# Kernel tuning notes

Hardware: AMD Instinct MI355X
Metric: run time of the kernel (lower is better)

Reference implementation:

```python
import jax, jax.numpy as jnp
import numpy as np

B, N, D = 8, 2048, 512


def setup_inputs() -> dict:
    key = jax.random.key(0)
    ks = jax.random.split(key, 8)
    s = 1.0 / np.sqrt(D)
    return {
        "x": jax.random.normal(ks[0], (B, N, D), dtype=jnp.float32),
        "event_lengths": jax.random.randint(ks[1], (B,), 1, N + 1, dtype=jnp.int64),
        "Wq": jax.random.uniform(ks[2], (D, D), jnp.float32, -s, s),
        "bq": jnp.zeros((D,), jnp.float32),
        "Wk": jax.random.uniform(ks[3], (D, D), jnp.float32, -s, s),
        "bk": jnp.zeros((D,), jnp.float32),
        "Wv": jax.random.uniform(ks[4], (D, D), jnp.float32, -s, s),
        "bv": jnp.zeros((D,), jnp.float32),
    }


def reference(x, event_lengths, Wq, bq, Wk, bk, Wv, bv):
    # x: [B, N, D]; linear layers follow torch convention y = x @ W^T + b
    q = jnp.einsum("bnd,ed->bne", x, Wq) + bq
    k = jnp.einsum("bnd,ed->bne", x, Wk) + bk
    v = jnp.einsum("bnd,ed->bne", x, Wv) + bv

    d = x.shape[-1]
    scores = jnp.einsum("bqd,bkd->bqk", q, k) / jnp.sqrt(jnp.asarray(d, jnp.float32))

    # per-sample padding mask: valid iff row < len AND col < len
    n = x.shape[1]
    idx = jnp.arange(n)
    L = event_lengths[:, None, None]  # [B,1,1]
    mask = (idx[None, :, None] < L) & (idx[None, None, :] < L)  # [B,N,N]
    scores = jnp.where(mask, scores, jnp.float32(-1e9))

    attn = jax.nn.softmax(scores, axis=-1)  # dropout omitted (eval mode)
    return jnp.einsum("bqk,bkd->bqd", attn, v)
```

## Files before the change

### kernel.cpp

```cpp
#include <hip/hip_runtime.h>

typedef _Float16 half8  __attribute__((ext_vector_type(8)));
typedef _Float16 half4  __attribute__((ext_vector_type(4)));
typedef _Float16 half2v __attribute__((ext_vector_type(2)));
typedef float    floatx4 __attribute__((ext_vector_type(4)));
typedef float    float4v __attribute__((ext_vector_type(4)));
typedef float    float2v __attribute__((ext_vector_type(2)));

#define BB 8
#define NN 2048
#define DD 512


#define WAITV(N)  asm volatile("s_waitcnt vmcnt(" #N ")" ::: "memory")
#define WAITL0()  asm volatile("s_waitcnt lgkmcnt(0)" ::: "memory")
#define BARRIER() asm volatile("s_barrier" ::: "memory")

__device__ __forceinline__ void stage_tile(const _Float16* __restrict__ g,
                                           int gstride, _Float16* lds,
                                           int w, int lane)
{
#pragma unroll
    for (int j = 0; j < 2; ++j) {
        int grp = w * 2 + j;
        int r   = grp * 16 + (lane >> 2);
        int cb  = (lane & 3) ^ ((r >> 1) & 3);
        const _Float16* gp = g + (size_t)r * gstride + cb * 8;
        _Float16* lp = lds + grp * 512;
        __builtin_amdgcn_global_load_lds(
            (const __attribute__((address_space(1))) void*)gp,
            (__attribute__((address_space(3))) void*)lp, 16, 0, 0);
    }
}

__device__ __forceinline__ void stage_tile64(const _Float16* __restrict__ g,
                                             int gstride, _Float16* lds,
                                             int w, int lane)
{
    int r  = w * 16 + (lane >> 2);
    int cb = (lane & 3) ^ ((r >> 1) & 3);
    const _Float16* gp = g + (size_t)r * gstride + cb * 8;
    _Float16* lp = lds + w * 512;
    __builtin_amdgcn_global_load_lds(
        (const __attribute__((address_space(1))) void*)gp,
        (__attribute__((address_space(3))) void*)lp, 16, 0, 0);
}

__device__ __forceinline__ half8 frag(const _Float16* tile, int m, int quad)
{
    return *(const half8*)&tile[m * 32 + ((quad ^ ((m >> 1) & 3)) * 8)];
}

__global__ __launch_bounds__(256) void prep_kernel(
    const float* __restrict__ x, const float* __restrict__ Wq,
    const float* __restrict__ Wk, const float* __restrict__ Wv,
    const int* __restrict__ lens,
    _Float16* __restrict__ xh, _Float16* __restrict__ wqh,
    _Float16* __restrict__ wkh, _Float16* __restrict__ wvh,
    float* __restrict__ sx)
{
    const int b  = blockIdx.y;
    const int n0 = blockIdx.x * 64;
    const int t  = threadIdx.x;
    const int Lp = (lens[b] + 127) & ~127;
    const float*   base  = x  + ((size_t)b * NN + n0) * DD + 2 * t;
    _Float16*      hbase = xh + ((size_t)b * NN + n0) * DD + 2 * t;

    int nw = Lp - n0;
    nw = nw < 0 ? 0 : (nw > 64 ? 64 : nw);

    float s0 = 0.f, s1 = 0.f;
    int n = 0;
    for (; n < nw; ++n) {
        float2v f = *(const float2v*)&base[(size_t)n * DD];
        s0 += f[0]; s1 += f[1];
        half2v h; h[0] = (_Float16)f[0]; h[1] = (_Float16)f[1];
        *(half2v*)&hbase[(size_t)n * DD] = h;
    }
    for (; n < 64; ++n) {
        float2v f = *(const float2v*)&base[(size_t)n * DD];
        s0 += f[0]; s1 += f[1];
    }
    atomicAdd(&sx[b * DD + 2 * t],     s0);
    atomicAdd(&sx[b * DD + 2 * t + 1], s1);

    const int gbid = b * 32 + blockIdx.x;
#pragma unroll
    for (int k = 0; k < 3; ++k) {
        int wi = gbid * 768 + k * 256 + t;
        const float* src; _Float16* dst; int i;
        if (wi < 65536)       { src = Wq; dst = wqh; i = wi; }
        else if (wi < 131072) { src = Wk; dst = wkh; i = wi - 65536; }
        else                  { src = Wv; dst = wvh; i = wi - 131072; }
        float4v f = *(const float4v*)&src[(size_t)i * 4];
        half4 h;
        for (int j = 0; j < 4; ++j) h[j] = (_Float16)f[j];
        *(half4*)&dst[(size_t)i * 4] = h;
    }
}

__global__ __launch_bounds__(256) void mvgemv_kernel(
    const float* __restrict__ Wv, const float* __restrict__ bv,
    const float* __restrict__ sx, float* __restrict__ mean_v)
{
    const int blk = blockIdx.x;
    const int b   = blk >> 7;
    const int e   = (blk & 127) * 4 + (threadIdx.x >> 6);
    const int lane = threadIdx.x & 63;
    const float* wr = Wv + (size_t)e * DD + lane * 8;
    const float* xr = sx + b * DD + lane * 8;
    float s = 0.f;
    for (int j = 0; j < 8; ++j) s += wr[j] * xr[j];
    for (int off = 32; off > 0; off >>= 1) s += __shfl_xor(s, off);
    if (lane == 0)
        mean_v[b * DD + e] = s * (1.0f / 2048.0f) + bv[e];
}

__global__ __launch_bounds__(256) void projqk_kernel(
    const _Float16* __restrict__ xh,
    const _Float16* __restrict__ wqh, const _Float16* __restrict__ wkh,
    const float* __restrict__ bq, const float* __restrict__ bk,
    const int* __restrict__ lens,
    _Float16* __restrict__ qb, _Float16* __restrict__ kb)
{
    const int z = blockIdx.z;
    const int r0 = blockIdx.y * 128;
    const int bb = r0 >> 11;
    if ((r0 & 2047) >= lens[bb]) return;
    const _Float16* Wh  = z ? wkh : wqh;
    const float*    bias= z ? bk  : bq;
    _Float16*       outp= z ? kb  : qb;
    const int c0 = blockIdx.x * 128;

    __shared__ __align__(16) _Float16 As[3][128 * 32];
    __shared__ __align__(16) _Float16 Bs[3][128 * 32];

    const int tid  = threadIdx.x;
    const int lane = tid & 63;
    const int w    = tid >> 6;
    const int wm   = w >> 1, wn = w & 1;
    const int lr   = lane & 15;
    const int quad = lane >> 4;

    floatx4 zero; zero[0]=0.f; zero[1]=0.f; zero[2]=0.f; zero[3]=0.f;
    floatx4 acc[4][4];
    for (int i = 0; i < 4; ++i)
        for (int j = 0; j < 4; ++j) acc[i][j] = zero;

    const _Float16* Abase = xh + (size_t)r0 * DD;
    const _Float16* Bbase = Wh + (size_t)c0 * DD;

    stage_tile(Abase +  0, DD, As[0], w, lane);
    stage_tile(Bbase +  0, DD, Bs[0], w, lane);
    stage_tile(Abase + 32, DD, As[1], w, lane);
    stage_tile(Bbase + 32, DD, Bs[1], w, lane);

    int cur = 0;
    for (int kt = 0; kt < 16; ++kt) {
        int nx = (kt + 2 < 16) ? kt + 2 : 15;
        int nb = cur + 2; if (nb >= 3) nb -= 3;
        stage_tile(Abase + nx * 32, DD, As[nb], w, lane);
        stage_tile(Bbase + nx * 32, DD, Bs[nb], w, lane);
        WAITV(8);
        BARRIER();
        half8 a[4], b[4];
        for (int mt = 0; mt < 4; ++mt) a[mt] = frag(As[cur], wm * 64 + mt * 16 + lr, quad);
        for (int nt = 0; nt < 4; ++nt) b[nt] = frag(Bs[cur], wn * 64 + nt * 16 + lr, quad);
        for (int mt = 0; mt < 4; ++mt)
            for (int nt = 0; nt < 4; ++nt)
                acc[mt][nt] = __builtin_amdgcn_mfma_f32_16x16x32_f16(a[mt], b[nt], acc[mt][nt], 0, 0, 0);
        WAITL0();
        BARRIER();
        cur = (cur + 1 == 3) ? 0 : cur + 1;
    }
    WAITV(0);

    for (int mt = 0; mt < 4; ++mt)
        for (int nt = 0; nt < 4; ++nt)
            for (int r = 0; r < 4; ++r) {
                int row = r0 + wm * 64 + mt * 16 + quad * 4 + r;
                int col = c0 + wn * 64 + nt * 16 + lr;
                outp[(size_t)row * DD + col] = (_Float16)(acc[mt][nt][r] + bias[col]);
            }
}

__global__ __launch_bounds__(256) void projv_kernel(
    const _Float16* __restrict__ xh,
    const _Float16* __restrict__ wvh, const float* __restrict__ bv,
    const int* __restrict__ lens, _Float16* __restrict__ vhT)
{
    const int b  = blockIdx.z;
    const int e0 = blockIdx.y * 128;
    const int n0 = blockIdx.x * 128;
    if (n0 >= lens[b]) return;

    __shared__ __align__(16) _Float16 As[3][128 * 32];
    __shared__ __align__(16) _Float16 Bs[3][128 * 32];

    const int tid  = threadIdx.x;
    const int lane = tid & 63;
    const int w    = tid >> 6;
    const int wm   = w >> 1, wn = w & 1;
    const int lr   = lane & 15;
    const int quad = lane >> 4;

    floatx4 zero; zero[0]=0.f; zero[1]=0.f; zero[2]=0.f; zero[3]=0.f;
    floatx4 acc[4][4];
    for (int i = 0; i < 4; ++i)
        for (int j = 0; j < 4; ++j) acc[i][j] = zero;

    const _Float16* Abase = wvh + (size_t)e0 * DD;
    const _Float16* Bbase = xh + ((size_t)b * NN + n0) * DD;

    stage_tile(Abase +  0, DD, As[0], w, lane);
    stage_tile(Bbase +  0, DD, Bs[0], w, lane);
    stage_tile(Abase + 32, DD, As[1], w, lane);
    stage_tile(Bbase + 32, DD, Bs[1], w, lane);

    int cur = 0;
    for (int kt = 0; kt < 16; ++kt) {
        int nx = (kt + 2 < 16) ? kt + 2 : 15;
        int nb = cur + 2; if (nb >= 3) nb -= 3;
        stage_tile(Abase + nx * 32, DD, As[nb], w, lane);
        stage_tile(Bbase + nx * 32, DD, Bs[nb], w, lane);
        WAITV(8);
        BARRIER();
        half8 a[4], bfr[4];
        for (int mt = 0; mt < 4; ++mt) a[mt]   = frag(As[cur], wm * 64 + mt * 16 + lr, quad);
        for (int nt = 0; nt < 4; ++nt) bfr[nt] = frag(Bs[cur], wn * 64 + nt * 16 + lr, quad);
        for (int mt = 0; mt < 4; ++mt)
            for (int nt = 0; nt < 4; ++nt)
                acc[mt][nt] = __builtin_amdgcn_mfma_f32_16x16x32_f16(a[mt], bfr[nt], acc[mt][nt], 0, 0, 0);
        WAITL0();
        BARRIER();
        cur = (cur + 1 == 3) ? 0 : cur + 1;
    }
    WAITV(0);

    for (int mt = 0; mt < 4; ++mt)
        for (int nt = 0; nt < 4; ++nt)
            for (int r = 0; r < 4; ++r) {
                int e = e0 + wm * 64 + mt * 16 + quad * 4 + r;
                int n = n0 + wn * 64 + nt * 16 + lr;
                vhT[((size_t)b * DD + e) * NN + n] = (_Float16)(acc[mt][nt][r] + bv[e]);
            }
}

__global__ __launch_bounds__(256) void scores_kernel(
    const _Float16* __restrict__ qb, const _Float16* __restrict__ kb,
    const int* __restrict__ lens, _Float16* __restrict__ S,
    float* __restrict__ rowsum)
{
    const int b  = blockIdx.z;
    const int r0 = blockIdx.y * 128;
    const int c0 = blockIdx.x * 128;
    const int L  = lens[b];
    if (r0 >= L || c0 >= L) return;
    const _Float16* Abase = qb + (size_t)b * NN * DD + (size_t)r0 * DD;
    const _Float16* Bbase = kb + (size_t)b * NN * DD + (size_t)c0 * DD;

    __shared__ __align__(16) _Float16 As[3][128 * 32];
    __shared__ __align__(16) _Float16 Bs[3][128 * 32];

    const int tid  = threadIdx.x;
    const int lane = tid & 63;
    const int w    = tid >> 6;
    const int wm   = w >> 1, wn = w & 1;
    const int lr   = lane & 15;
    const int quad = lane >> 4;

    floatx4 zero; zero[0]=0.f; zero[1]=0.f; zero[2]=0.f; zero[3]=0.f;
    floatx4 acc[4][4];
    for (int i = 0; i < 4; ++i)
        for (int j = 0; j < 4; ++j) acc[i][j] = zero;

    stage_tile(Abase +  0, DD, As[0], w, lane);
    stage_tile(Bbase +  0, DD, Bs[0], w, lane);
    stage_tile(Abase + 32, DD, As[1], w, lane);
    stage_tile(Bbase + 32, DD, Bs[1], w, lane);

    int cur = 0;
    for (int kt = 0; kt < 16; ++kt) {
        int nx = (kt + 2 < 16) ? kt + 2 : 15;
        int nb = cur + 2; if (nb >= 3) nb -= 3;
        stage_tile(Abase + nx * 32, DD, As[nb], w, lane);
        stage_tile(Bbase + nx * 32, DD, Bs[nb], w, lane);
        WAITV(8);
        BARRIER();
        half8 a[4], bfr[4];
        for (int mt = 0; mt < 4; ++mt) a[mt]   = frag(As[cur], wm * 64 + mt * 16 + lr, quad);
        for (int nt = 0; nt < 4; ++nt) bfr[nt] = frag(Bs[cur], wn * 64 + nt * 16 + lr, quad);
        for (int mt = 0; mt < 4; ++mt)
            for (int nt = 0; nt < 4; ++nt)
                acc[mt][nt] = __builtin_amdgcn_mfma_f32_16x16x32_f16(a[mt], bfr[nt], acc[mt][nt], 0, 0, 0);
        WAITL0();
        BARRIER();
        cur = (cur + 1 == 3) ? 0 : cur + 1;
    }
    WAITV(0);

    const float scale = 0.044194173824159216f;
    float psum[4][4];
    for (int mt = 0; mt < 4; ++mt)
        for (int r = 0; r < 4; ++r) psum[mt][r] = 0.f;

    for (int mt = 0; mt < 4; ++mt)
        for (int nt = 0; nt < 4; ++nt)
            for (int r = 0; r < 4; ++r) {
                int q    = r0 + wm * 64 + mt * 16 + quad * 4 + r;
                int kcol = c0 + wn * 64 + nt * 16 + lr;
                float e  = (kcol < L) ? __expf(acc[mt][nt][r] * scale) : 0.f;
                psum[mt][r] += e;
                S[((size_t)b * NN + q) * NN + kcol] = (_Float16)e;
            }

    for (int mt = 0; mt < 4; ++mt)
        for (int r = 0; r < 4; ++r) {
            float s = psum[mt][r];
            s += __shfl_xor(s, 1);
            s += __shfl_xor(s, 2);
            s += __shfl_xor(s, 4);
            s += __shfl_xor(s, 8);
            if (lr == 0) {
                int q = r0 + wm * 64 + mt * 16 + quad * 4 + r;
                if (q < L) atomicAdd(&rowsum[b * NN + q], s);
            }
        }
}

__global__ __launch_bounds__(256) void pv_kernel(
    const _Float16* __restrict__ P, const _Float16* __restrict__ vhT,
    const int* __restrict__ lens, const float* __restrict__ mean_v,
    const float* __restrict__ rowsum, float* __restrict__ out)
{
    const int b  = blockIdx.z;
    const int L  = lens[b];
    const int r0 = blockIdx.y * 64;
    const int c0 = blockIdx.x * 128;
    const int KT = (r0 < L) ? ((L + 31) >> 5) : 0;
    const _Float16* A  = P   + (size_t)b * NN * NN + (size_t)r0 * NN;
    const _Float16* Vh = vhT + (size_t)b * DD * NN + (size_t)c0 * NN;

    __shared__ __align__(16) _Float16 As[2][64 * 32];
    __shared__ __align__(16) _Float16 Bhs[2][128 * 32];

    const int tid  = threadIdx.x;
    const int lane = tid & 63;
    const int w    = tid >> 6;
    const int lr   = lane & 15;
    const int quad = lane >> 4;

    floatx4 zero; zero[0]=0.f; zero[1]=0.f; zero[2]=0.f; zero[3]=0.f;
    floatx4 acc[4][2];
    for (int i = 0; i < 4; ++i)
        for (int j = 0; j < 2; ++j) acc[i][j] = zero;

    if (KT > 0) {
        stage_tile64(A, NN, As[0], w, lane);
        stage_tile (Vh, NN, Bhs[0], w, lane);
    }
    for (int kt = 0; kt < KT; ++kt) {
        const int cur = kt & 1;
        __syncthreads();
        if (kt + 1 < KT) {
            stage_tile64(A + (size_t)(kt + 1) * 32, NN, As[cur ^ 1], w, lane);
            stage_tile (Vh + (size_t)(kt + 1) * 32, NN, Bhs[cur ^ 1], w, lane);
        }
        half8 a[4], bh[2];
        for (int mt = 0; mt < 4; ++mt) a[mt]  = frag(As[cur], mt * 16 + lr, quad);
        for (int nt = 0; nt < 2; ++nt) bh[nt] = frag(Bhs[cur], w * 32 + nt * 16 + lr, quad);
        for (int mt = 0; mt < 4; ++mt)
            for (int nt = 0; nt < 2; ++nt)
                acc[mt][nt] = __builtin_amdgcn_mfma_f32_16x16x32_f16(a[mt], bh[nt], acc[mt][nt], 0, 0, 0);
    }

    float mval[2];
    for (int nt = 0; nt < 2; ++nt)
        mval[nt] = mean_v[b * DD + c0 + w * 32 + nt * 16 + lr];

    for (int mt = 0; mt < 4; ++mt)
        for (int r = 0; r < 4; ++r) {
            int q = r0 + mt * 16 + quad * 4 + r;
            float inv = 0.f;
            if (q < L) inv = 1.0f / rowsum[b * NN + q];
            for (int nt = 0; nt < 2; ++nt) {
                int e = c0 + w * 32 + nt * 16 + lr;
                float val = (q < L) ? acc[mt][nt][r] * inv : mval[nt];
                out[((size_t)b * NN + q) * DD + e] = val;
            }
        }
}

extern "C" void kernel_launch(void* const* d_in, const int* in_sizes, int n_in,
                              void* d_out, int out_size, void* d_ws, size_t ws_size,
                              hipStream_t stream) {
    const float* x    = (const float*)d_in[0];
    const int*   lens = (const int*)d_in[1];
    const float* Wq   = (const float*)d_in[2];
    const float* bq   = (const float*)d_in[3];
    const float* Wk   = (const float*)d_in[4];
    const float* bk   = (const float*)d_in[5];
    const float* Wv   = (const float*)d_in[6];
    const float* bv   = (const float*)d_in[7];
    float* out = (float*)d_out;

    char* ws = (char*)d_ws;
    const size_t MB = 1024 * 1024;
    _Float16* qb  = (_Float16*)(ws);
    _Float16* kb  = (_Float16*)(ws + 16 * MB);
    _Float16* vh  = (_Float16*)(ws + 32 * MB);
    float*    mv  = (float*)   (ws + 48 * MB);
    float*    sx  = (float*)   (ws + 48 * MB + 64 * 1024);
    float*    rs  = (float*)   (ws + 48 * MB + 80 * 1024);
    _Float16* S   = (_Float16*)(ws + 64 * MB);
    _Float16* xh  = (_Float16*)(ws + 64 * MB);
    _Float16* wqh = (_Float16*)(ws + 80 * MB);
    _Float16* wkh = (_Float16*)(ws + 80 * MB + 512 * 1024);
    _Float16* wvh = (_Float16*)(ws + 81 * MB);

    hipMemsetAsync(sx, 0, BB * DD * sizeof(float) + BB * NN * sizeof(float), stream);
    prep_kernel  <<<dim3(32, 8),     256, 0, stream>>>(x, Wq, Wk, Wv, lens, xh, wqh, wkh, wvh, sx);
    mvgemv_kernel<<<1024,            256, 0, stream>>>(Wv, bv, sx, mv);
    projqk_kernel<<<dim3(4, 128, 2), 256, 0, stream>>>(xh, wqh, wkh, bq, bk, lens, qb, kb);
    projv_kernel <<<dim3(16, 4, 8),  256, 0, stream>>>(xh, wvh, bv, lens, vh);
    scores_kernel<<<dim3(16, 16, 8), 256, 0, stream>>>(qb, kb, lens, S, rs);
    pv_kernel    <<<dim3(4, 32, 8),  256, 0, stream>>>(S, vh, lens, mv, rs, out);
}
```

Baseline: 235.6 us.

## Split prep into flat cast and mean kernels, halve PV row tile

The fused prep kernel is split into a flat elementwise fp16 cast kernel over x and the weights, plus a separate column-sum kernel for the mean of x. Both spread across many more threads. The PV kernel row tile drops from 64 to 32 and the grid doubles, which raises parallelism for short sequences at the cost of re-reading V tiles more often. The scores epilogue is reorganised to keep the row-sum partials per m-tile, lowering register pressure. Because the cast and the mean each read x separately, x is now read twice from memory.

```diff
diff --git a/kernel.cpp b/kernel.cpp
--- a/kernel.cpp
+++ b/kernel.cpp
@@ -2,10 +2,8 @@
 
 typedef _Float16 half8  __attribute__((ext_vector_type(8)));
 typedef _Float16 half4  __attribute__((ext_vector_type(4)));
-typedef _Float16 half2v __attribute__((ext_vector_type(2)));
 typedef float    floatx4 __attribute__((ext_vector_type(4)));
 typedef float    float4v __attribute__((ext_vector_type(4)));
-typedef float    float2v __attribute__((ext_vector_type(2)));
 
 #define BB 8
 #define NN 2048
@@ -33,7 +31,7 @@
     }
 }
 
-__device__ __forceinline__ void stage_tile64(const _Float16* __restrict__ g,
+__device__ __forceinline__ void stage_tile16(const _Float16* __restrict__ g,
                                              int gstride, _Float16* lds,
                                              int w, int lane)
 {
@@ -56,47 +54,42 @@
     const float* __restrict__ Wk, const float* __restrict__ Wv,
     const int* __restrict__ lens,
     _Float16* __restrict__ xh, _Float16* __restrict__ wqh,
-    _Float16* __restrict__ wkh, _Float16* __restrict__ wvh,
-    float* __restrict__ sx)
+    _Float16* __restrict__ wkh, _Float16* __restrict__ wvh)
+{
+    const int XQ = (BB * NN * DD) / 4;
+    const int WQ = (DD * DD) / 4;
+    int t = blockIdx.x * 256 + threadIdx.x;
+    const float* src; _Float16* dst; int i;
+    if (t < XQ) {
+        int row = t >> 7;
+        int b   = row >> 11;
+        if ((row & 2047) >= ((lens[b] + 127) & ~127)) return;
+        src = x;  dst = xh;  i = t;
+    }
+    else if (t < XQ + WQ)   { src = Wq; dst = wqh; i = t - XQ; }
+    else if (t < XQ + 2*WQ) { src = Wk; dst = wkh; i = t - XQ - WQ; }
+    else if (t < XQ + 3*WQ) { src = Wv; dst = wvh; i = t - XQ - 2*WQ; }
+    else return;
+    float4v f = *(const float4v*)&src[(size_t)i * 4];
+    half4 h;
+    for (int j = 0; j < 4; ++j) h[j] = (_Float16)f[j];
+    *(half4*)&dst[(size_t)i * 4] = h;
+}
+
+__global__ __launch_bounds__(256) void meanx_kernel(
+    const float* __restrict__ x, float* __restrict__ sx)
 {
     const int b  = blockIdx.y;
     const int n0 = blockIdx.x * 64;
-    const int t  = threadIdx.x;
-    const int Lp = (lens[b] + 127) & ~127;
-    const float*   base  = x  + ((size_t)b * NN + n0) * DD + 2 * t;
-    _Float16*      hbase = xh + ((size_t)b * NN + n0) * DD + 2 * t;
-
-    int nw = Lp - n0;
-    nw = nw < 0 ? 0 : (nw > 64 ? 64 : nw);
-
+    const int d0 = threadIdx.x;
     float s0 = 0.f, s1 = 0.f;
-    int n = 0;
-    for (; n < nw; ++n) {
-        float2v f = *(const float2v*)&base[(size_t)n * DD];
-        s0 += f[0]; s1 += f[1];
-        half2v h; h[0] = (_Float16)f[0]; h[1] = (_Float16)f[1];
-        *(half2v*)&hbase[(size_t)n * DD] = h;
-    }
-    for (; n < 64; ++n) {
-        float2v f = *(const float2v*)&base[(size_t)n * DD];
-        s0 += f[0]; s1 += f[1];
-    }
-    atomicAdd(&sx[b * DD + 2 * t],     s0);
-    atomicAdd(&sx[b * DD + 2 * t + 1], s1);
-
-    const int gbid = b * 32 + blockIdx.x;
-#pragma unroll
-    for (int k = 0; k < 3; ++k) {
-        int wi = gbid * 768 + k * 256 + t;
-        const float* src; _Float16* dst; int i;
-        if (wi < 65536)       { src = Wq; dst = wqh; i = wi; }
-        else if (wi < 131072) { src = Wk; dst = wkh; i = wi - 65536; }
-        else                  { src = Wv; dst = wvh; i = wi - 131072; }
-        float4v f = *(const float4v*)&src[(size_t)i * 4];
-        half4 h;
-        for (int j = 0; j < 4; ++j) h[j] = (_Float16)f[j];
-        *(half4*)&dst[(size_t)i * 4] = h;
-    }
+    const float* base = x + ((size_t)b * NN + n0) * DD;
+    for (int n = 0; n < 64; ++n) {
+        s0 += base[n * DD + d0];
+        s1 += base[n * DD + d0 + 256];
+    }
+    atomicAdd(&sx[b * DD + d0], s0);
+    atomicAdd(&sx[b * DD + d0 + 256], s1);
 }
 
 __global__ __launch_bounds__(256) void mvgemv_kernel(
@@ -300,23 +293,20 @@
     WAITV(0);
 
     const float scale = 0.044194173824159216f;
-    float psum[4][4];
-    for (int mt = 0; mt < 4; ++mt)
-        for (int r = 0; r < 4; ++r) psum[mt][r] = 0.f;
-
-    for (int mt = 0; mt < 4; ++mt)
-        for (int nt = 0; nt < 4; ++nt)
+    for (int mt = 0; mt < 4; ++mt) {
+        float psum[4] = {0.f, 0.f, 0.f, 0.f};
+        for (int nt = 0; nt < 4; ++nt) {
+            int kcol = c0 + wn * 64 + nt * 16 + lr;
+            float em = (kcol < L) ? 1.f : 0.f;
             for (int r = 0; r < 4; ++r) {
                 int q    = r0 + wm * 64 + mt * 16 + quad * 4 + r;
-                int kcol = c0 + wn * 64 + nt * 16 + lr;
-                float e  = (kcol < L) ? __expf(acc[mt][nt][r] * scale) : 0.f;
-                psum[mt][r] += e;
+                float e  = em * __expf(acc[mt][nt][r] * scale);
+                psum[r] += e;
                 S[((size_t)b * NN + q) * NN + kcol] = (_Float16)e;
             }
-
-    for (int mt = 0; mt < 4; ++mt)
+        }
         for (int r = 0; r < 4; ++r) {
-            float s = psum[mt][r];
+            float s = psum[r];
             s += __shfl_xor(s, 1);
             s += __shfl_xor(s, 2);
             s += __shfl_xor(s, 4);
@@ -326,6 +316,7 @@
                 if (q < L) atomicAdd(&rowsum[b * NN + q], s);
             }
         }
+    }
 }
 
 __global__ __launch_bounds__(256) void pv_kernel(
@@ -335,13 +326,13 @@
 {
     const int b  = blockIdx.z;
     const int L  = lens[b];
-    const int r0 = blockIdx.y * 64;
+    const int r0 = blockIdx.y * 32;
     const int c0 = blockIdx.x * 128;
     const int KT = (r0 < L) ? ((L + 31) >> 5) : 0;
     const _Float16* A  = P   + (size_t)b * NN * NN + (size_t)r0 * NN;
     const _Float16* Vh = vhT + (size_t)b * DD * NN + (size_t)c0 * NN;
 
-    __shared__ __align__(16) _Float16 As[2][64 * 32];
+    __shared__ __align__(16) _Float16 As[2][32 * 32];
     __shared__ __align__(16) _Float16 Bhs[2][128 * 32];
 
     const int tid  = threadIdx.x;
@@ -351,25 +342,25 @@
     const int quad = lane >> 4;
 
     floatx4 zero; zero[0]=0.f; zero[1]=0.f; zero[2]=0.f; zero[3]=0.f;
-    floatx4 acc[4][2];
-    for (int i = 0; i < 4; ++i)
+    floatx4 acc[2][2];
+    for (int i = 0; i < 2; ++i)
         for (int j = 0; j < 2; ++j) acc[i][j] = zero;
 
     if (KT > 0) {
-        stage_tile64(A, NN, As[0], w, lane);
-        stage_tile (Vh, NN, Bhs[0], w, lane);
+        if (w < 2) stage_tile16(A, NN, As[0], w, lane);
+        stage_tile(Vh, NN, Bhs[0], w, lane);
     }
     for (int kt = 0; kt < KT; ++kt) {
         const int cur = kt & 1;
         __syncthreads();
         if (kt + 1 < KT) {
-            stage_tile64(A + (size_t)(kt + 1) * 32, NN, As[cur ^ 1], w, lane);
-            stage_tile (Vh + (size_t)(kt + 1) * 32, NN, Bhs[cur ^ 1], w, lane);
+            if (w < 2) stage_tile16(A + (size_t)(kt + 1) * 32, NN, As[cur ^ 1], w, lane);
+            stage_tile(Vh + (size_t)(kt + 1) * 32, NN, Bhs[cur ^ 1], w, lane);
         }
-        half8 a[4], bh[2];
-        for (int mt = 0; mt < 4; ++mt) a[mt]  = frag(As[cur], mt * 16 + lr, quad);
+        half8 a[2], bh[2];
+        for (int mt = 0; mt < 2; ++mt) a[mt]  = frag(As[cur], mt * 16 + lr, quad);
         for (int nt = 0; nt < 2; ++nt) bh[nt] = frag(Bhs[cur], w * 32 + nt * 16 + lr, quad);
-        for (int mt = 0; mt < 4; ++mt)
+        for (int mt = 0; mt < 2; ++mt)
             for (int nt = 0; nt < 2; ++nt)
                 acc[mt][nt] = __builtin_amdgcn_mfma_f32_16x16x32_f16(a[mt], bh[nt], acc[mt][nt], 0, 0, 0);
     }
@@ -378,7 +369,7 @@
     for (int nt = 0; nt < 2; ++nt)
         mval[nt] = mean_v[b * DD + c0 + w * 32 + nt * 16 + lr];
 
-    for (int mt = 0; mt < 4; ++mt)
+    for (int mt = 0; mt < 2; ++mt)
         for (int r = 0; r < 4; ++r) {
             int q = r0 + mt * 16 + quad * 4 + r;
             float inv = 0.f;
@@ -419,10 +410,11 @@
     _Float16* wvh = (_Float16*)(ws + 81 * MB);
 
     hipMemsetAsync(sx, 0, BB * DD * sizeof(float) + BB * NN * sizeof(float), stream);
-    prep_kernel  <<<dim3(32, 8),     256, 0, stream>>>(x, Wq, Wk, Wv, lens, xh, wqh, wkh, wvh, sx);
+    prep_kernel  <<<8960,            256, 0, stream>>>(x, Wq, Wk, Wv, lens, xh, wqh, wkh, wvh);
+    meanx_kernel <<<dim3(32, 8),     256, 0, stream>>>(x, sx);
     mvgemv_kernel<<<1024,            256, 0, stream>>>(Wv, bv, sx, mv);
     projqk_kernel<<<dim3(4, 128, 2), 256, 0, stream>>>(xh, wqh, wkh, bq, bk, lens, qb, kb);
     projv_kernel <<<dim3(16, 4, 8),  256, 0, stream>>>(xh, wvh, bv, lens, vh);
     scores_kernel<<<dim3(16, 16, 8), 256, 0, stream>>>(qb, kb, lens, S, rs);
-    pv_kernel    <<<dim3(4, 32, 8),  256, 0, stream>>>(S, vh, lens, mv, rs, out);
-}
+    pv_kernel    <<<dim3(4, 64, 8),  256, 0, stream>>>(S, vh, lens, mv, rs, out);
+}
```

Result: faster. 215.3 us (-8.6%).
